# Performance work log

Hardware: AMD Instinct MI355X
Metric: run time of the kernel (lower is better)

The kernel has to match this reference:

```python
import jax, jax.numpy as jnp
import numpy as np

N_NODES = 100000
N_EDGES = 3200000
IN_FEATS = 128
H_FEATS = 256
REG_NUM = 1


def _linear_params(key, fan_in, fan_out):
    kw, kb = jax.random.split(key)
    bound = 1.0 / np.sqrt(fan_in)
    W = jax.random.uniform(kw, (fan_out, fan_in), minval=-bound, maxval=bound, dtype=jnp.float32)
    b = jax.random.uniform(kb, (fan_out,), minval=-bound, maxval=bound, dtype=jnp.float32)
    return W, b


def setup_inputs() -> dict:
    key = jax.random.key(0)
    ks = jax.random.split(key, 12)
    node_feat = jax.random.normal(ks[0], (N_NODES, IN_FEATS), dtype=jnp.float32)
    edge_feat = jax.random.normal(ks[1], (N_EDGES, 1), dtype=jnp.float32)
    edge_dst = jax.random.randint(ks[2], (N_EDGES,), 0, N_NODES, dtype=jnp.int64)
    # SAGE layer weights: conv1 maps in_feats+1 -> h_feats; mids map h_feats+1 -> h_feats
    W1, b1 = _linear_params(ks[3], IN_FEATS + 1, H_FEATS)
    Wm1, bm1 = _linear_params(ks[4], H_FEATS + 1, H_FEATS)
    Wm2, bm2 = _linear_params(ks[5], H_FEATS + 1, H_FEATS)
    Wm3, bm3 = _linear_params(ks[6], H_FEATS + 1, H_FEATS)
    Wm4, bm4 = _linear_params(ks[7], H_FEATS + 1, H_FEATS)
    Wr1, br1 = _linear_params(ks[8], H_FEATS + 1, H_FEATS)
    Wr2, br2 = _linear_params(ks[9], H_FEATS, H_FEATS)
    Wr3, br3 = _linear_params(ks[10], H_FEATS, REG_NUM)
    return {
        "node_feat": node_feat, "edge_feat": edge_feat, "edge_dst": edge_dst,
        "W1": W1, "b1": b1,
        "Wm1": Wm1, "bm1": bm1, "Wm2": Wm2, "bm2": bm2,
        "Wm3": Wm3, "bm3": bm3, "Wm4": Wm4, "bm4": bm4,
        "Wr1": Wr1, "br1": br1, "Wr2": Wr2, "br2": br2, "Wr3": Wr3, "br3": br3,
    }


def _sage_layer(hn, he_aggr, W, b):
    # concat [N, d] with [N, 1] then linear
    h_total = jnp.concatenate([hn, he_aggr], axis=1)
    return h_total @ W.T + b


def reference(node_feat, edge_feat, edge_dst,
              W1, b1, Wm1, bm1, Wm2, bm2, Wm3, bm3, Wm4, bm4,
              Wr1, br1, Wr2, br2, Wr3, br3):
    # copy_e + sum: scatter-add edge features onto destination nodes -> [N, 1]
    he_aggr = jax.ops.segment_sum(edge_feat, edge_dst, num_segments=N_NODES)
    h = jax.nn.relu(_sage_layer(node_feat, he_aggr, W1, b1))  # dropout = identity (eval)
    h = jax.nn.relu(_sage_layer(h, he_aggr, Wm1, bm1))
    h = jax.nn.relu(_sage_layer(h, he_aggr, Wm2, bm2))
    h = jax.nn.relu(_sage_layer(h, he_aggr, Wm3, bm3))
    h = jax.nn.relu(_sage_layer(h, he_aggr, Wm4, bm4))
    h = jax.nn.relu(_sage_layer(h, he_aggr, Wr1, br1))
    h = jax.nn.relu(h @ Wr2.T + br2)
    return h @ Wr3.T + br3
```

## Files before the change

kernel.cpp:

```cpp
#include <hip/hip_runtime.h>
#include <hip/hip_bf16.h>

typedef _Float16 half8  __attribute__((ext_vector_type(8)));
typedef _Float16 half4v __attribute__((ext_vector_type(4)));
typedef float    f32x4  __attribute__((ext_vector_type(4)));

#define N_NODES 100000
#define N_EDGES 3200000
#define SH_STRIDE 100096
#define NBUCK 782
#define CAP   5120
#define CHUNK 16384
#define NBIN  196
#define NPK   16

__global__ __launch_bounds__(1024) void binpack(
    const float* __restrict__ ef, const int* __restrict__ dst,
    const float* __restrict__ W1,  const float* __restrict__ Wm1,
    const float* __restrict__ Wm2, const float* __restrict__ Wm3,
    const float* __restrict__ Wm4, const float* __restrict__ Wr1,
    const float* __restrict__ Wr2,
    const float* __restrict__ b1,  const float* __restrict__ bm1,
    const float* __restrict__ bm2, const float* __restrict__ bm3,
    const float* __restrict__ bm4, const float* __restrict__ br1,
    const float* __restrict__ br2, const float* __restrict__ wr3,
    const float* __restrict__ br3,
    int* __restrict__ cursor, unsigned* __restrict__ pairs,
    _Float16* __restrict__ Wp, float* __restrict__ park, int do_bin) {

    if (do_bin && blockIdx.x < NBIN) {
        __shared__ int hist[NBUCK];
        __shared__ int base[NBUCK];
        const int start = blockIdx.x * CHUNK;
        const int end   = min(start + CHUNK, N_EDGES);
        const int tid   = threadIdx.x;
        for (int b = tid; b < NBUCK; b += 1024) hist[b] = 0;
        __syncthreads();

        int4   dreg[4];
        float4 freg[4];
        #pragma unroll
        for (int it = 0; it < 4; ++it) {
            const int i = start + it * 4096 + tid * 4;
            if (i < end) {
                dreg[it] = *(const int4*)&dst[i];
                freg[it] = *(const float4*)&ef[i];
                atomicAdd(&hist[dreg[it].x >> 7], 1);
                atomicAdd(&hist[dreg[it].y >> 7], 1);
                atomicAdd(&hist[dreg[it].z >> 7], 1);
                atomicAdd(&hist[dreg[it].w >> 7], 1);
            }
        }
        __syncthreads();
        for (int b = tid; b < NBUCK; b += 1024) {
            const int c = hist[b];
            base[b] = b * CAP + ((c > 0) ? atomicAdd(&cursor[b], c) : 0);
            hist[b] = 0;
        }
        __syncthreads();
        #pragma unroll
        for (int it = 0; it < 4; ++it) {
            const int i = start + it * 4096 + tid * 4;
            if (i < end) {
                const int4   d = dreg[it];
                const float4 f = freg[it];
                {   const int bk = d.x >> 7;
                    const int s  = base[bk] + atomicAdd(&hist[bk], 1);
                    if (s < bk * CAP + CAP)
                        pairs[s] = (__float_as_uint(f.x) & 0xFFFFFF00u) | (unsigned)(d.x & 127); }
                {   const int bk = d.y >> 7;
                    const int s  = base[bk] + atomicAdd(&hist[bk], 1);
                    if (s < bk * CAP + CAP)
                        pairs[s] = (__float_as_uint(f.y) & 0xFFFFFF00u) | (unsigned)(d.y & 127); }
                {   const int bk = d.z >> 7;
                    const int s  = base[bk] + atomicAdd(&hist[bk], 1);
                    if (s < bk * CAP + CAP)
                        pairs[s] = (__float_as_uint(f.z) & 0xFFFFFF00u) | (unsigned)(d.z & 127); }
                {   const int bk = d.w >> 7;
                    const int s  = base[bk] + atomicAdd(&hist[bk], 1);
                    if (s < bk * CAP + CAP)
                        pairs[s] = (__float_as_uint(f.w) & 0xFFFFFF00u) | (unsigned)(d.w & 127); }
            }
        }
    } else {
        const float* srcs[7] = {W1, Wm1, Wm2, Wm3, Wm4, Wr1, Wr2};
        const float* bias[7] = {b1, bm1, bm2, bm3, bm4, br1, br2};
        const int pb  = do_bin ? ((int)blockIdx.x - NBIN) : (int)blockIdx.x;
        const int gid = pb * 1024 + threadIdx.x;
        const int gsz = NPK * 1024;
        for (int i = gid; i < 425984; i += gsz) {
            int job, row, k, stride;
            if (i < 32768) { job = 0; row = i >> 7; k = i & 127; stride = 129; }
            else {
                int t = i - 32768; job = 1 + (t >> 16); int w = t & 65535;
                row = w >> 8; k = w & 255; stride = (job == 6) ? 256 : 257;
            }
            Wp[i] = (_Float16)srcs[job][row * stride + k];
        }
        for (int i = gid; i < 1536; i += gsz) {
            const int job = i >> 8, row = i & 255;
            const int stride = (job == 0) ? 129 : 257;
            const int kin    = (job == 0) ? 128 : 256;
            park[job * 512 + row] = srcs[job][row * stride + kin];
        }
        for (int i = gid; i < 256; i += gsz) park[6 * 512 + i] = 0.f;
        for (int i = gid; i < 1792; i += gsz)
            park[(i >> 8) * 512 + 256 + (i & 255)] = bias[i >> 8][i & 255];
        for (int i = gid; i < 256; i += gsz) park[3584 + i] = wr3[i];
        if (gid == 0) park[3840] = br3[0];
    }
}

__global__ void scatter4(const float4* __restrict__ ef4,
                         const int4* __restrict__ dst4,
                         float* __restrict__ e) {
    const int n4 = N_EDGES / 4;
    for (int i = blockIdx.x * blockDim.x + threadIdx.x; i < n4;
         i += gridDim.x * blockDim.x) {
        const float4 f = ef4[i];
        const int4   d = dst4[i];
        atomicAdd(&e[d.x], f.x);
        atomicAdd(&e[SH_STRIDE + d.y], f.y);
        atomicAdd(&e[2 * SH_STRIDE + d.z], f.z);
        atomicAdd(&e[3 * SH_STRIDE + d.w], f.w);
    }
}

template<int K>
__device__ __forceinline__ void layer_mm(const _Float16* __restrict__ Wl,
                                         _Float16 (* __restrict__ Hs)[264],
                                         const float* __restrict__ es,
                                         const float* __restrict__ parkl,
                                         int wave, int m_, int quad) {
    f32x4 acc[4][8];
    #pragma unroll
    for (int jt = 0; jt < 4; ++jt)
        #pragma unroll
        for (int mt = 0; mt < 8; ++mt)
            acc[jt][mt] = (f32x4){0.f, 0.f, 0.f, 0.f};

    const int jb0 = wave * 64 + quad * 4;
    float4 w4[4], bb[4];
    #pragma unroll
    for (int jt = 0; jt < 4; ++jt) {
        w4[jt] = *(const float4*)&parkl[jt * 16 + jb0];
        bb[jt] = *(const float4*)&parkl[256 + jt * 16 + jb0];
    }

    const _Float16* __restrict__ wp = Wl + (size_t)(wave * 64 + m_) * K + quad * 8;

    half8 a[4];
    #pragma unroll
    for (int jt = 0; jt < 4; ++jt)
        a[jt] = *(const half8*)(wp + jt * 16 * K);

    #pragma unroll
    for (int kk = 0; kk < K; kk += 32) {
        half8 a2[4];
        if (kk + 32 < K) {
            #pragma unroll
            for (int jt = 0; jt < 4; ++jt)
                a2[jt] = *(const half8*)(wp + jt * 16 * K + kk + 32);
        }
        half8 b[8];
        #pragma unroll
        for (int mt = 0; mt < 8; ++mt)
            b[mt] = *(const half8*)&Hs[mt * 16 + m_][kk + quad * 8];
        #pragma unroll
        for (int jt = 0; jt < 4; ++jt)
            #pragma unroll
            for (int mt = 0; mt < 8; ++mt)
                acc[jt][mt] = __builtin_amdgcn_mfma_f32_16x16x32_f16(
                    a[jt], b[mt], acc[jt][mt], 0, 0, 0);
        if (kk + 32 < K) {
            #pragma unroll
            for (int jt = 0; jt < 4; ++jt) a[jt] = a2[jt];
        }
    }
    __syncthreads();

    #pragma unroll
    for (int jt = 0; jt < 4; ++jt) {
        const int jbase = jb0 + jt * 16;
        #pragma unroll
        for (int mt = 0; mt < 8; ++mt) {
            const int node = mt * 16 + m_;
            const float ev = es[node];
            half4v h;
            h[0] = (_Float16)fmaxf(acc[jt][mt][0] + ev * w4[jt].x + bb[jt].x, 0.f);
            h[1] = (_Float16)fmaxf(acc[jt][mt][1] + ev * w4[jt].y + bb[jt].y, 0.f);
            h[2] = (_Float16)fmaxf(acc[jt][mt][2] + ev * w4[jt].z + bb[jt].z, 0.f);
            h[3] = (_Float16)fmaxf(acc[jt][mt][3] + ev * w4[jt].w + bb[jt].w, 0.f);
            *(half4v*)&Hs[node][jbase] = h;
        }
    }
    __syncthreads();
}

__global__ __launch_bounds__(256, 2) void sage_fused(
    const float* __restrict__ node_feat,
    const int* __restrict__ cursor, const unsigned* __restrict__ pairs,
    const float* __restrict__ esh, int nsh,
    const _Float16* __restrict__ Wpack, const float* __restrict__ park,
    float* __restrict__ out) {

    __shared__ _Float16 Hs[128][264];
    __shared__ float es[128];
    __shared__ float wf[256];
    __shared__ float red[2][128];

    const int tid  = threadIdx.x;
    const int wave = tid >> 6;
    const int lane = tid & 63;
    const int m_   = lane & 15;
    const int quad = lane >> 4;
    const int node0 = blockIdx.x * 128;

    if (tid < 128) es[tid] = 0.f;
    __syncthreads();

    for (int idx = tid; idx < 128 * 16; idx += 256) {
        const int row = idx >> 4, g = idx & 15;
        int node = node0 + row; if (node >= N_NODES) node = N_NODES - 1;
        const float4* src = (const float4*)(node_feat + (size_t)node * 128 + g * 8);
        const float4 v0 = src[0], v1 = src[1];
        half8 h;
        h[0] = (_Float16)v0.x; h[1] = (_Float16)v0.y;
        h[2] = (_Float16)v0.z; h[3] = (_Float16)v0.w;
        h[4] = (_Float16)v1.x; h[5] = (_Float16)v1.y;
        h[6] = (_Float16)v1.z; h[7] = (_Float16)v1.w;
        *(half8*)&Hs[row][g * 8] = h;
    }
    if (nsh == 0) {
        const int cnt = min(cursor[blockIdx.x], CAP);
        const unsigned* __restrict__ pp = pairs + (size_t)blockIdx.x * CAP;
        for (int i = tid; i < cnt; i += 256) {
            const unsigned p = pp[i];
            atomicAdd(&es[p & 127u], __uint_as_float(p & 0xFFFFFF00u));
        }
    } else if (tid < 128) {
        int node = node0 + tid; if (node >= N_NODES) node = N_NODES - 1;
        float s = 0.f;
        for (int sh = 0; sh < nsh; ++sh) s += esh[(size_t)sh * SH_STRIDE + node];
        es[tid] = s;
    }
    __syncthreads();

    layer_mm<128>(Wpack, Hs, es, park, wave, m_, quad);
    for (int l = 1; l < 7; ++l)
        layer_mm<256>(Wpack + 32768 + (l - 1) * 65536, Hs, es, park + l * 512,
                      wave, m_, quad);

    wf[tid] = park[3584 + tid];
    __syncthreads();
    {
        const int row = tid & 127, seg = tid >> 7;
        const _Float16* hp = &Hs[row][seg * 128];
        const float* wpt = &wf[seg * 128];
        float s = 0.f;
        #pragma unroll 8
        for (int k = 0; k < 128; ++k) s += (float)hp[k] * wpt[k];
        red[seg][row] = s;
    }
    __syncthreads();
    if (tid < 128) {
        const int node = node0 + tid;
        if (node < N_NODES)
            out[node] = red[0][tid] + red[1][tid] + park[3840];
    }
}

extern "C" void kernel_launch(void* const* d_in, const int* in_sizes, int n_in,
                              void* d_out, int out_size, void* d_ws,
                              size_t ws_size, hipStream_t stream) {
    const float* node_feat = (const float*)d_in[0];
    const float* edge_feat = (const float*)d_in[1];
    const int*   edge_dst  = (const int*)d_in[2];
    const float* W1  = (const float*)d_in[3];  const float* b1  = (const float*)d_in[4];
    const float* Wm1 = (const float*)d_in[5];  const float* bm1 = (const float*)d_in[6];
    const float* Wm2 = (const float*)d_in[7];  const float* bm2 = (const float*)d_in[8];
    const float* Wm3 = (const float*)d_in[9];  const float* bm3 = (const float*)d_in[10];
    const float* Wm4 = (const float*)d_in[11]; const float* bm4 = (const float*)d_in[12];
    const float* Wr1 = (const float*)d_in[13]; const float* br1 = (const float*)d_in[14];
    const float* Wr2 = (const float*)d_in[15]; const float* br2 = (const float*)d_in[16];
    const float* Wr3 = (const float*)d_in[17]; const float* br3 = (const float*)d_in[18];
    float* out = (float*)d_out;

    char* ws = (char*)d_ws;
    int*      cursor = (int*)ws;
    _Float16* Wp     = (_Float16*)(ws + 4096);
    float*    park   = (float*)(ws + 856064);
    unsigned* pairs  = (unsigned*)(ws + 872448);
    float*    esh    = (float*)(ws + 872448);

    const size_t need_bins = 872448 + (size_t)NBUCK * CAP * 4;
    const bool use_bins = (ws_size >= need_bins);

    const int nblk = (N_NODES + 127) / 128;

    if (use_bins) {
        hipMemsetAsync(cursor, 0, NBUCK * sizeof(int), stream);
        binpack<<<NBIN + NPK, 1024, 0, stream>>>(
            edge_feat, edge_dst, W1, Wm1, Wm2, Wm3, Wm4, Wr1, Wr2,
            b1, bm1, bm2, bm3, bm4, br1, br2, Wr3, br3,
            cursor, pairs, Wp, park, 1);
        sage_fused<<<nblk, 256, 0, stream>>>(node_feat, cursor, pairs,
                                             nullptr, 0, Wp, park, out);
    } else {
        binpack<<<NPK, 1024, 0, stream>>>(
            edge_feat, edge_dst, W1, Wm1, Wm2, Wm3, Wm4, Wr1, Wr2,
            b1, bm1, bm2, bm3, bm4, br1, br2, Wr3, br3,
            cursor, pairs, Wp, park, 0);
        hipMemsetAsync(esh, 0, (size_t)4 * SH_STRIDE * 4, stream);
        scatter4<<<3125, 256, 0, stream>>>((const float4*)edge_feat,
                                           (const int4*)edge_dst, esh);
        sage_fused<<<nblk, 256, 0, stream>>>(node_feat, nullptr, nullptr,
                                             esh, 4, Wp, park, out);
    }
}
```

Measured before the change: 294.6 us.

## Stage binned edge records in LDS sorted by bucket before global scatter

The binning kernel now does a block-wide prefix scan over bucket counts, writes each edge record into a bucket-sorted local LDS buffer, and then writes the records to global memory in that sorted order. Consecutive threads write into contiguous slots of the same bucket, which is meant to replace the random scattered global stores with more coalesced ones. The chunk size drops to 12288 so the LDS staging buffers fit, giving more bin blocks. The added scan costs about 20 barriers per block, and the sage_fused kernel's minimum-blocks-per-CU launch bound is removed, which may change its register allocation.

```diff
diff --git a/kernel.cpp b/kernel.cpp
--- a/kernel.cpp
+++ b/kernel.cpp
@@ -10,8 +10,8 @@
 #define SH_STRIDE 100096
 #define NBUCK 782
 #define CAP   5120
-#define CHUNK 16384
-#define NBIN  196
+#define CHUNK 12288
+#define NBIN  261
 #define NPK   16
 
 __global__ __launch_bounds__(1024) void binpack(
@@ -29,20 +29,23 @@
     _Float16* __restrict__ Wp, float* __restrict__ park, int do_bin) {
 
     if (do_bin && blockIdx.x < NBIN) {
-        __shared__ int hist[NBUCK];
-        __shared__ int base[NBUCK];
+        __shared__ int      hist[NBUCK];
+        __shared__ int      base[NBUCK];
+        __shared__ int      scan[1024];
+        __shared__ int      lbase[NBUCK];
+        __shared__ unsigned lrec[CHUNK];
+        __shared__ int      lslot[CHUNK];
         const int start = blockIdx.x * CHUNK;
-        const int end   = min(start + CHUNK, N_EDGES);
         const int tid   = threadIdx.x;
         for (int b = tid; b < NBUCK; b += 1024) hist[b] = 0;
         __syncthreads();
 
-        int4   dreg[4];
-        float4 freg[4];
-        #pragma unroll
-        for (int it = 0; it < 4; ++it) {
-            const int i = start + it * 4096 + tid * 4;
-            if (i < end) {
+        int4   dreg[3];
+        float4 freg[3];
+        #pragma unroll
+        for (int it = 0; it < 3; ++it) {
+            const int i = start + (it * 1024 + tid) * 4;
+            if (i < N_EDGES) {
                 dreg[it] = *(const int4*)&dst[i];
                 freg[it] = *(const float4*)&ef[i];
                 atomicAdd(&hist[dreg[it].x >> 7], 1);
@@ -52,35 +55,55 @@
             }
         }
         __syncthreads();
-        for (int b = tid; b < NBUCK; b += 1024) {
-            const int c = hist[b];
-            base[b] = b * CAP + ((c > 0) ? atomicAdd(&cursor[b], c) : 0);
-            hist[b] = 0;
-        }
-        __syncthreads();
-        #pragma unroll
-        for (int it = 0; it < 4; ++it) {
-            const int i = start + it * 4096 + tid * 4;
-            if (i < end) {
+        if (tid < NBUCK) {
+            const int c = hist[tid];
+            base[tid] = tid * CAP + ((c > 0) ? atomicAdd(&cursor[tid], c) : 0);
+            scan[tid] = c;
+        } else {
+            scan[tid] = 0;
+        }
+        __syncthreads();
+        #pragma unroll
+        for (int ofs = 1; ofs < 1024; ofs <<= 1) {
+            const int v = (tid >= ofs) ? scan[tid - ofs] : 0;
+            __syncthreads();
+            scan[tid] += v;
+            __syncthreads();
+        }
+        if (tid < NBUCK) {
+            lbase[tid] = scan[tid] - hist[tid];
+            hist[tid]  = 0;
+        }
+        __syncthreads();
+        #pragma unroll
+        for (int it = 0; it < 3; ++it) {
+            const int i = start + (it * 1024 + tid) * 4;
+            if (i < N_EDGES) {
                 const int4   d = dreg[it];
                 const float4 f = freg[it];
-                {   const int bk = d.x >> 7;
-                    const int s  = base[bk] + atomicAdd(&hist[bk], 1);
-                    if (s < bk * CAP + CAP)
-                        pairs[s] = (__float_as_uint(f.x) & 0xFFFFFF00u) | (unsigned)(d.x & 127); }
-                {   const int bk = d.y >> 7;
-                    const int s  = base[bk] + atomicAdd(&hist[bk], 1);
-                    if (s < bk * CAP + CAP)
-                        pairs[s] = (__float_as_uint(f.y) & 0xFFFFFF00u) | (unsigned)(d.y & 127); }
-                {   const int bk = d.z >> 7;
-                    const int s  = base[bk] + atomicAdd(&hist[bk], 1);
-                    if (s < bk * CAP + CAP)
-                        pairs[s] = (__float_as_uint(f.z) & 0xFFFFFF00u) | (unsigned)(d.z & 127); }
-                {   const int bk = d.w >> 7;
-                    const int s  = base[bk] + atomicAdd(&hist[bk], 1);
-                    if (s < bk * CAP + CAP)
-                        pairs[s] = (__float_as_uint(f.w) & 0xFFFFFF00u) | (unsigned)(d.w & 127); }
+                {   const int bk = d.x >> 7; const int r = atomicAdd(&hist[bk], 1);
+                    const int s = lbase[bk] + r; const int g = base[bk] + r;
+                    lrec[s]  = (__float_as_uint(f.x) & 0xFFFFFF00u) | (unsigned)(d.x & 127);
+                    lslot[s] = (g < (bk + 1) * CAP) ? g : -1; }
+                {   const int bk = d.y >> 7; const int r = atomicAdd(&hist[bk], 1);
+                    const int s = lbase[bk] + r; const int g = base[bk] + r;
+                    lrec[s]  = (__float_as_uint(f.y) & 0xFFFFFF00u) | (unsigned)(d.y & 127);
+                    lslot[s] = (g < (bk + 1) * CAP) ? g : -1; }
+                {   const int bk = d.z >> 7; const int r = atomicAdd(&hist[bk], 1);
+                    const int s = lbase[bk] + r; const int g = base[bk] + r;
+                    lrec[s]  = (__float_as_uint(f.z) & 0xFFFFFF00u) | (unsigned)(d.z & 127);
+                    lslot[s] = (g < (bk + 1) * CAP) ? g : -1; }
+                {   const int bk = d.w >> 7; const int r = atomicAdd(&hist[bk], 1);
+                    const int s = lbase[bk] + r; const int g = base[bk] + r;
+                    lrec[s]  = (__float_as_uint(f.w) & 0xFFFFFF00u) | (unsigned)(d.w & 127);
+                    lslot[s] = (g < (bk + 1) * CAP) ? g : -1; }
             }
+        }
+        __syncthreads();
+        const int total = min(CHUNK, N_EDGES - start);
+        for (int s = tid; s < total; s += 1024) {
+            const int g = lslot[s];
+            if (g >= 0) pairs[g] = lrec[s];
         }
     } else {
         const float* srcs[7] = {W1, Wm1, Wm2, Wm3, Wm4, Wr1, Wr2};
@@ -197,7 +220,7 @@
     __syncthreads();
 }
 
-__global__ __launch_bounds__(256, 2) void sage_fused(
+__global__ __launch_bounds__(256) void sage_fused(
     const float* __restrict__ node_feat,
     const int* __restrict__ cursor, const unsigned* __restrict__ pairs,
     const float* __restrict__ esh, int nsh,
```

New measurement: 330.8 us. 1.12x slower.

## Replace atomic bucket cursors with histogram, scan, and deterministic placement passes

Applied to the files above, without the earlier changes.

The single binning kernel, which reserved per-bucket slots through global atomics on a shared cursor array, is split into three kernels. A histogram pass writes per-chunk bucket counts, a single-block scan turns them into per-chunk offsets and bucket totals, and a placement pass re-reads the edges and writes the packed pairs. This removes the global atomic contention and the memset and makes placement order deterministic. In exchange it adds two kernel launches, a second read of edge_dst, and a serial scan of 196 rows run by one block.

```diff
diff --git a/kernel.cpp b/kernel.cpp
--- a/kernel.cpp
+++ b/kernel.cpp
@@ -14,8 +14,8 @@
 #define NBIN  196
 #define NPK   16
 
-__global__ __launch_bounds__(1024) void binpack(
-    const float* __restrict__ ef, const int* __restrict__ dst,
+__global__ __launch_bounds__(1024) void hist_pack(
+    const int* __restrict__ dst,
     const float* __restrict__ W1,  const float* __restrict__ Wm1,
     const float* __restrict__ Wm2, const float* __restrict__ Wm3,
     const float* __restrict__ Wm4, const float* __restrict__ Wr1,
@@ -25,63 +25,29 @@
     const float* __restrict__ bm4, const float* __restrict__ br1,
     const float* __restrict__ br2, const float* __restrict__ wr3,
     const float* __restrict__ br3,
-    int* __restrict__ cursor, unsigned* __restrict__ pairs,
-    _Float16* __restrict__ Wp, float* __restrict__ park, int do_bin) {
+    int* __restrict__ counts, _Float16* __restrict__ Wp,
+    float* __restrict__ park, int do_bin) {
 
     if (do_bin && blockIdx.x < NBIN) {
         __shared__ int hist[NBUCK];
-        __shared__ int base[NBUCK];
+        const int tid   = threadIdx.x;
         const int start = blockIdx.x * CHUNK;
-        const int end   = min(start + CHUNK, N_EDGES);
-        const int tid   = threadIdx.x;
         for (int b = tid; b < NBUCK; b += 1024) hist[b] = 0;
         __syncthreads();
-
-        int4   dreg[4];
-        float4 freg[4];
         #pragma unroll
         for (int it = 0; it < 4; ++it) {
-            const int i = start + it * 4096 + tid * 4;
-            if (i < end) {
-                dreg[it] = *(const int4*)&dst[i];
-                freg[it] = *(const float4*)&ef[i];
-                atomicAdd(&hist[dreg[it].x >> 7], 1);
-                atomicAdd(&hist[dreg[it].y >> 7], 1);
-                atomicAdd(&hist[dreg[it].z >> 7], 1);
-                atomicAdd(&hist[dreg[it].w >> 7], 1);
+            const int i = start + (it * 1024 + tid) * 4;
+            if (i < N_EDGES) {
+                const int4 d = *(const int4*)&dst[i];
+                atomicAdd(&hist[d.x >> 7], 1);
+                atomicAdd(&hist[d.y >> 7], 1);
+                atomicAdd(&hist[d.z >> 7], 1);
+                atomicAdd(&hist[d.w >> 7], 1);
             }
         }
         __syncthreads();
-        for (int b = tid; b < NBUCK; b += 1024) {
-            const int c = hist[b];
-            base[b] = b * CAP + ((c > 0) ? atomicAdd(&cursor[b], c) : 0);
-            hist[b] = 0;
-        }
-        __syncthreads();
-        #pragma unroll
-        for (int it = 0; it < 4; ++it) {
-            const int i = start + it * 4096 + tid * 4;
-            if (i < end) {
-                const int4   d = dreg[it];
-                const float4 f = freg[it];
-                {   const int bk = d.x >> 7;
-                    const int s  = base[bk] + atomicAdd(&hist[bk], 1);
-                    if (s < bk * CAP + CAP)
-                        pairs[s] = (__float_as_uint(f.x) & 0xFFFFFF00u) | (unsigned)(d.x & 127); }
-                {   const int bk = d.y >> 7;
-                    const int s  = base[bk] + atomicAdd(&hist[bk], 1);
-                    if (s < bk * CAP + CAP)
-                        pairs[s] = (__float_as_uint(f.y) & 0xFFFFFF00u) | (unsigned)(d.y & 127); }
-                {   const int bk = d.z >> 7;
-                    const int s  = base[bk] + atomicAdd(&hist[bk], 1);
-                    if (s < bk * CAP + CAP)
-                        pairs[s] = (__float_as_uint(f.z) & 0xFFFFFF00u) | (unsigned)(d.z & 127); }
-                {   const int bk = d.w >> 7;
-                    const int s  = base[bk] + atomicAdd(&hist[bk], 1);
-                    if (s < bk * CAP + CAP)
-                        pairs[s] = (__float_as_uint(f.w) & 0xFFFFFF00u) | (unsigned)(d.w & 127); }
-            }
-        }
+        int* __restrict__ row = counts + (size_t)blockIdx.x * NBUCK;
+        for (int b = tid; b < NBUCK; b += 1024) row[b] = hist[b];
     } else {
         const float* srcs[7] = {W1, Wm1, Wm2, Wm3, Wm4, Wr1, Wr2};
         const float* bias[7] = {b1, bm1, bm2, bm3, bm4, br1, br2};
@@ -111,6 +77,53 @@
     }
 }
 
+__global__ __launch_bounds__(1024) void scan_k(int* __restrict__ counts,
+                                               int* __restrict__ cnt) {
+    const int t = threadIdx.x;
+    if (t < NBUCK) {
+        int run = 0;
+        #pragma unroll 4
+        for (int j = 0; j < NBIN; ++j) {
+            const int c = counts[(size_t)j * NBUCK + t];
+            counts[(size_t)j * NBUCK + t] = run;
+            run += c;
+        }
+        cnt[t] = run;
+    }
+}
+
+__global__ __launch_bounds__(1024) void place_k(
+    const float* __restrict__ ef, const int* __restrict__ dst,
+    const int* __restrict__ counts, unsigned* __restrict__ pairs) {
+    __shared__ int basel[NBUCK];
+    __shared__ int hist[NBUCK];
+    const int tid   = threadIdx.x;
+    const int start = blockIdx.x * CHUNK;
+    const int* __restrict__ row = counts + (size_t)blockIdx.x * NBUCK;
+    for (int b = tid; b < NBUCK; b += 1024) { basel[b] = row[b]; hist[b] = 0; }
+    __syncthreads();
+    #pragma unroll
+    for (int it = 0; it < 4; ++it) {
+        const int i = start + (it * 1024 + tid) * 4;
+        if (i < N_EDGES) {
+            const int4   d = *(const int4*)&dst[i];
+            const float4 f = *(const float4*)&ef[i];
+            {   const int bk = d.x >> 7; const int s = basel[bk] + atomicAdd(&hist[bk], 1);
+                if (s < CAP) pairs[(size_t)bk * CAP + s] =
+                    (__float_as_uint(f.x) & 0xFFFFFF00u) | (unsigned)(d.x & 127); }
+            {   const int bk = d.y >> 7; const int s = basel[bk] + atomicAdd(&hist[bk], 1);
+                if (s < CAP) pairs[(size_t)bk * CAP + s] =
+                    (__float_as_uint(f.y) & 0xFFFFFF00u) | (unsigned)(d.y & 127); }
+            {   const int bk = d.z >> 7; const int s = basel[bk] + atomicAdd(&hist[bk], 1);
+                if (s < CAP) pairs[(size_t)bk * CAP + s] =
+                    (__float_as_uint(f.z) & 0xFFFFFF00u) | (unsigned)(d.z & 127); }
+            {   const int bk = d.w >> 7; const int s = basel[bk] + atomicAdd(&hist[bk], 1);
+                if (s < CAP) pairs[(size_t)bk * CAP + s] =
+                    (__float_as_uint(f.w) & 0xFFFFFF00u) | (unsigned)(d.w & 127); }
+        }
+    }
+}
+
 __global__ void scatter4(const float4* __restrict__ ef4,
                          const int4* __restrict__ dst4,
                          float* __restrict__ e) {
@@ -199,7 +212,7 @@
 
 __global__ __launch_bounds__(256, 2) void sage_fused(
     const float* __restrict__ node_feat,
-    const int* __restrict__ cursor, const unsigned* __restrict__ pairs,
+    const int* __restrict__ cnt, const unsigned* __restrict__ pairs,
     const float* __restrict__ esh, int nsh,
     const _Float16* __restrict__ Wpack, const float* __restrict__ park,
     float* __restrict__ out) {
@@ -232,9 +245,9 @@
         *(half8*)&Hs[row][g * 8] = h;
     }
     if (nsh == 0) {
-        const int cnt = min(cursor[blockIdx.x], CAP);
+        const int c = min(cnt[blockIdx.x], CAP);
         const unsigned* __restrict__ pp = pairs + (size_t)blockIdx.x * CAP;
-        for (int i = tid; i < cnt; i += 256) {
+        for (int i = tid; i < c; i += 256) {
             const unsigned p = pp[i];
             atomicAdd(&es[p & 127u], __uint_as_float(p & 0xFFFFFF00u));
         }
@@ -287,30 +300,32 @@
     float* out = (float*)d_out;
 
     char* ws = (char*)d_ws;
-    int*      cursor = (int*)ws;
-    _Float16* Wp     = (_Float16*)(ws + 4096);
-    float*    park   = (float*)(ws + 856064);
-    unsigned* pairs  = (unsigned*)(ws + 872448);
-    float*    esh    = (float*)(ws + 872448);
-
-    const size_t need_bins = 872448 + (size_t)NBUCK * CAP * 4;
+    _Float16* Wp     = (_Float16*)ws;
+    float*    park   = (float*)(ws + 851968);
+    int*      counts = (int*)(ws + 868352);
+    int*      cnt    = (int*)(ws + 1481440);
+    unsigned* pairs  = (unsigned*)(ws + 1484800);
+    float*    esh    = (float*)(ws + 1484800);
+
+    const size_t need_bins = 1484800 + (size_t)NBUCK * CAP * 4;
     const bool use_bins = (ws_size >= need_bins);
 
     const int nblk = (N_NODES + 127) / 128;
 
     if (use_bins) {
-        hipMemsetAsync(cursor, 0, NBUCK * sizeof(int), stream);
-        binpack<<<NBIN + NPK, 1024, 0, stream>>>(
-            edge_feat, edge_dst, W1, Wm1, Wm2, Wm3, Wm4, Wr1, Wr2,
+        hist_pack<<<NBIN + NPK, 1024, 0, stream>>>(
+            edge_dst, W1, Wm1, Wm2, Wm3, Wm4, Wr1, Wr2,
             b1, bm1, bm2, bm3, bm4, br1, br2, Wr3, br3,
-            cursor, pairs, Wp, park, 1);
-        sage_fused<<<nblk, 256, 0, stream>>>(node_feat, cursor, pairs,
+            counts, Wp, park, 1);
+        scan_k<<<1, 1024, 0, stream>>>(counts, cnt);
+        place_k<<<NBIN, 1024, 0, stream>>>(edge_feat, edge_dst, counts, pairs);
+        sage_fused<<<nblk, 256, 0, stream>>>(node_feat, cnt, pairs,
                                              nullptr, 0, Wp, park, out);
     } else {
-        binpack<<<NPK, 1024, 0, stream>>>(
-            edge_feat, edge_dst, W1, Wm1, Wm2, Wm3, Wm4, Wr1, Wr2,
+        hist_pack<<<NPK, 1024, 0, stream>>>(
+            edge_dst, W1, Wm1, Wm2, Wm3, Wm4, Wr1, Wr2,
             b1, bm1, bm2, bm3, bm4, br1, br2, Wr3, br3,
-            cursor, pairs, Wp, park, 0);
+            counts, Wp, park, 0);
         hipMemsetAsync(esh, 0, (size_t)4 * SH_STRIDE * 4, stream);
         scatter4<<<3125, 256, 0, stream>>>((const float4*)edge_feat,
                                            (const int4*)edge_dst, esh);
```

Result: slower. 316.3 us (+7.4%).
